# Performance work log

Hardware: AMD Instinct MI355X
Metric: run time of the kernel (lower is better)

## Reference

```python
import jax, jax.numpy as jnp
import numpy as np

B, N, L = 64, 256, 2048
COMP, PROT, GAT, HEADS, LATENT = 128, 128, 64, 4, 128
N_ATOM, N_AMINO = 100, 25
WINDOW, LAYER_CNN, LAYER_OUT = 5, 3, 3
ALPHA = 0.2
BIDAT = 4


def _lrelu(x, s=ALPHA):
    return jax.nn.leaky_relu(x, negative_slope=s)


def _gat(h, adj_pos, W, a, concat):
    # e[b,i,j] = leakyrelu(a1.Wh_i + a2.Wh_j): avoids the O(N^2,2F) concat tensor.
    Wh = h @ W                      # [B,N,F]
    F = W.shape[1]
    f1 = Wh @ a[:F]                 # [B,N]
    f2 = Wh @ a[F:]                 # [B,N]
    e = _lrelu(f1[:, :, None] + f2[:, None, :])          # [B,N,N]
    att = jax.nn.softmax(jnp.where(adj_pos, e, -9e15), axis=2)
    hp = att @ Wh                   # [B,N,F]
    return jax.nn.elu(hp) if concat else hp


def _mask_softmax(a, mask):
    e = jnp.exp(a - jnp.max(a, axis=-1, keepdims=True)) * mask
    return e / (jnp.sum(e, axis=-1, keepdims=True) + 1e-6)


def _forward(atoms, atoms_mask, adjacency, amino, amino_mask, fps, inv_Temp, Temp,
             E_atom, E_amino, gatW, gatA, goW, goA, Wc_w, Wc_b, conv_k, conv_b,
             Wp_w, Wp_b, fp0, fp1, U, t_c2p_w, t_c2p_b, t_p2c_w, t_p2c_b,
             bh_c_w, bh_c_b, bh_p_w, bh_p_b, ba_c_w, ba_c_b, ba_p_w, ba_p_b,
             comb_c_w, comb_c_b, comb_p_w, comb_p_b, Wout_w, Wout_b, out_w, out_b):
    adj_pos = adjacency > 0
    # ---- comp_gat ----
    av = E_atom[atoms]                                   # [B,N,COMP]
    mh = jnp.concatenate([_gat(av, adj_pos, gatW[i], gatA[i], True) for i in range(HEADS)], axis=2)
    av = jax.nn.elu(_gat(mh, adj_pos, goW, goA, False))
    av = _lrelu(av @ Wc_w + Wc_b)                        # [B,N,LATENT]
    # ---- prot_cnn ----
    pv = E_amino[amino][:, None]                         # [B,1,L,PROT]
    for i in range(LAYER_CNN):
        pv = _lrelu(jax.lax.conv_general_dilated(
            pv, conv_k[i][None, None], (1, 1),
            [(WINDOW, WINDOW), (WINDOW, WINDOW)],
            dimension_numbers=("NCHW", "OIHW", "NCHW")) + conv_b[i])
    pv = _lrelu(pv[:, 0] @ Wp_w + Wp_b)                  # [B,L,LATENT]
    # ---- fingerprint superfeature ----
    sf = _lrelu(_lrelu(fps @ fp0, 0.1) @ fp1, 0.1)       # [B,LATENT]
    # ---- bidirectional attention ----
    cfs, pfs = [], []
    for i in range(BIDAT):
        A = jnp.tanh(jnp.einsum("bnd,de,bme->bnm", av, U[i], pv))   # [B,N,L]
        A = A * (atoms_mask[:, :, None] * amino_mask[:, None, :])
        atoms_trans = A @ jnp.tanh(pv @ t_p2c_w[i] + t_p2c_b[i])     # [B,N,LATENT]
        amino_trans = jnp.einsum("bnm,bnd->bmd", A, jnp.tanh(av @ t_c2p_w[i] + t_c2p_b[i]))
        atoms_tmp = jnp.concatenate([jnp.tanh(av @ bh_c_w[i] + bh_c_b[i]), atoms_trans], axis=2)
        amino_tmp = jnp.concatenate([jnp.tanh(pv @ bh_p_w[i] + bh_p_b[i]), amino_trans], axis=2)
        a_att = _mask_softmax((atoms_tmp @ ba_c_w[i] + ba_c_b[i])[..., 0], atoms_mask)
        p_att = _mask_softmax((amino_tmp @ ba_p_w[i] + ba_p_b[i])[..., 0], amino_mask)
        cfs.append(jnp.sum(av * a_att[:, :, None], axis=1))
        pfs.append(jnp.sum(pv * p_att[:, :, None], axis=1))
    cf_final = jnp.concatenate([jnp.concatenate(cfs, axis=1) @ comb_c_w + comb_c_b, sf], axis=1)
    pf_final = jnp.concatenate(pfs, axis=1) @ comb_p_w + comb_p_b
    v = jnp.concatenate([cf_final, pf_final, inv_Temp, Temp], axis=1)   # [B,3*LATENT+2]
    for j in range(LAYER_OUT):
        v = _lrelu(v @ Wout_w[j] + Wout_b[j])
    return v @ out_w + out_b                             # [B,1]


def setup_inputs() -> dict:
    key = jax.random.key(0)
    ks = iter(jax.random.split(key, 48))
    def nrm(shape, scale=0.1):
        return jax.random.normal(next(ks), shape, jnp.float32) * scale
    inp = {}
    inp["atoms"] = jax.random.randint(next(ks), (B, N), 0, N_ATOM)
    inp["atoms_mask"] = jnp.ones((B, N), jnp.float32)
    inp["adjacency"] = jax.random.randint(next(ks), (B, N, N), 0, 2).astype(jnp.int32)
    inp["amino"] = jax.random.randint(next(ks), (B, L), 0, N_AMINO)
    inp["amino_mask"] = jnp.ones((B, L), jnp.float32)
    inp["fps"] = jax.random.uniform(next(ks), (B, 1024), jnp.float32)
    inp["inv_Temp"] = jax.random.uniform(next(ks), (B, 1), jnp.float32)
    inp["Temp"] = jax.random.uniform(next(ks), (B, 1), jnp.float32)
    inp["E_atom"] = nrm((N_ATOM + 1, COMP))
    inp["E_amino"] = nrm((N_AMINO + 1, PROT))
    inp["gatW"] = nrm((HEADS, COMP, GAT))
    inp["gatA"] = nrm((HEADS, 2 * GAT))
    inp["goW"] = nrm((GAT * HEADS, COMP))
    inp["goA"] = nrm((2 * COMP,))
    inp["Wc_w"] = nrm((COMP, LATENT)); inp["Wc_b"] = nrm((LATENT,))
    K = 2 * WINDOW + 1
    inp["conv_k"] = nrm((LAYER_CNN, K, K)); inp["conv_b"] = nrm((LAYER_CNN,))
    inp["Wp_w"] = nrm((PROT, LATENT)); inp["Wp_b"] = nrm((LATENT,))
    inp["fp0"] = nrm((1024, LATENT)); inp["fp1"] = nrm((LATENT, LATENT))
    inp["U"] = nrm((BIDAT, LATENT, LATENT))
    inp["t_c2p_w"] = nrm((BIDAT, LATENT, LATENT)); inp["t_c2p_b"] = nrm((BIDAT, LATENT))
    inp["t_p2c_w"] = nrm((BIDAT, LATENT, LATENT)); inp["t_p2c_b"] = nrm((BIDAT, LATENT))
    inp["bh_c_w"] = nrm((BIDAT, LATENT, LATENT)); inp["bh_c_b"] = nrm((BIDAT, LATENT))
    inp["bh_p_w"] = nrm((BIDAT, LATENT, LATENT)); inp["bh_p_b"] = nrm((BIDAT, LATENT))
    inp["ba_c_w"] = nrm((BIDAT, 2 * LATENT, 1)); inp["ba_c_b"] = nrm((BIDAT, 1))
    inp["ba_p_w"] = nrm((BIDAT, 2 * LATENT, 1)); inp["ba_p_b"] = nrm((BIDAT, 1))
    inp["comb_c_w"] = nrm((BIDAT * LATENT, LATENT)); inp["comb_c_b"] = nrm((LATENT,))
    inp["comb_p_w"] = nrm((BIDAT * LATENT, LATENT)); inp["comb_p_b"] = nrm((LATENT,))
    D = 3 * LATENT + 2
    inp["Wout_w"] = nrm((LAYER_OUT, D, D)); inp["Wout_b"] = nrm((LAYER_OUT, D))
    inp["out_w"] = nrm((D, 1)); inp["out_b"] = nrm((1,))
    return inp


def reference(atoms, atoms_mask, adjacency, amino, amino_mask, fps, inv_Temp, Temp,
              E_atom, E_amino, gatW, gatA, goW, goA, Wc_w, Wc_b, conv_k, conv_b,
              Wp_w, Wp_b, fp0, fp1, U, t_c2p_w, t_c2p_b, t_p2c_w, t_p2c_b,
              bh_c_w, bh_c_b, bh_p_w, bh_p_b, ba_c_w, ba_c_b, ba_p_w, ba_p_b,
              comb_c_w, comb_c_b, comb_p_w, comb_p_b, Wout_w, Wout_b, out_w, out_b):
    return _forward(atoms, atoms_mask, adjacency, amino, amino_mask, fps, inv_Temp, Temp,
                    E_atom, E_amino, gatW, gatA, goW, goA, Wc_w, Wc_b, conv_k, conv_b,
                    Wp_w, Wp_b, fp0, fp1, U, t_c2p_w, t_c2p_b, t_p2c_w, t_p2c_b,
                    bh_c_w, bh_c_b, bh_p_w, bh_p_b, ba_c_w, ba_c_b, ba_p_w, ba_p_b,
                    comb_c_w, comb_c_b, comb_p_w, comb_p_b, Wout_w, Wout_b, out_w, out_b)
```

## Files before the change

### kernel.cpp

```cpp
#include <hip/hip_runtime.h>
#include <math.h>

#define Bn   64
#define Nn   256
#define Ln   2048
#define CMP  128
#define PROT 128
#define GF   64
#define NHEADS 4
#define LT   128
#define DOUT 386
#define CB   32
#define NCH  (Bn / CB)
#define FLSP 4

typedef unsigned short u16;
typedef unsigned long long u64;
typedef __attribute__((ext_vector_type(8))) short short8v;
typedef __attribute__((ext_vector_type(4))) float f32x4;
typedef __attribute__((ext_vector_type(4))) unsigned short u16x4;
typedef __attribute__((ext_vector_type(4))) unsigned int u32x4;

#define MFMA(a, b, c) __builtin_amdgcn_mfma_f32_16x16x32_bf16((a), (b), (c), 0, 0, 0)

__device__ __forceinline__ float apply_act(float v, int act) {
  if (act == 1) return v > 0.f ? v : 0.2f * v;
  if (act == 2) return v > 0.f ? v : 0.1f * v;
  if (act == 3) return tanhf(v);
  return v;
}

__device__ __forceinline__ u16 bfc(float f) {
  union { float f; unsigned u; } x; x.f = f;
  unsigned r = x.u + 0x7fffu + ((x.u >> 16) & 1u);
  return (u16)(r >> 16);
}

__device__ __forceinline__ float bf2f(u16 h) {
  union { unsigned u; float f; } x; x.u = ((unsigned)h) << 16; return x.f;
}

__device__ __forceinline__ float ftanh(float x) {
  float e = __builtin_amdgcn_exp2f(x * 2.885390081777927f);
  return 1.f - 2.f * __builtin_amdgcn_rcpf(e + 1.f);
}

template<int C>
__device__ __forceinline__ int lofs(int r, int c) {
  if (C == 256) return ((r * C + c) * 2) ^ ((r & 15) << 4);
  if (C == 128) return ((r * C + c) * 2) ^ ((r & 15) << 4);
  return ((r * C + c) * 2) ^ ((r & 7) << 4);
}

__device__ __forceinline__ short8v ldsv(const u16* s, int byteofs) {
  return *(const short8v*)((const char*)s + byteofs);
}

__global__ void embed_kernel(const int* __restrict__ idx, const float* __restrict__ E,
                             float* __restrict__ out, long total, int C) {
  long i = (long)blockIdx.x * blockDim.x + threadIdx.x;
  if (i >= total) return;
  long r = i / C;
  int c = (int)(i - r * (long)C);
  out[i] = E[(long)idx[r] * C + c];
}

__global__ void zero_kernel(float* __restrict__ a, long n) {
  long i = (long)blockIdx.x * blockDim.x + threadIdx.x;
  if (i < n) a[i] = 0.f;
}

__global__ void packadj_kernel(const int* __restrict__ adj, u64* __restrict__ adjb) {
  long idx = (long)blockIdx.x * 256 + threadIdx.x;
  int lane = threadIdx.x & 63;
  bool bit = adj[idx] > 0;
  u64 m = __ballot(bit);
  if (lane == 0) adjb[idx >> 6] = m;
}

__global__ void transp_kernel(const float* __restrict__ src, u16* __restrict__ dst,
                              int K, int N) {
  long total = (long)K * N;
  long base = (long)blockIdx.y * total;
  long idx = (long)blockIdx.x * 256 + threadIdx.x;
  if (idx >= total) return;
  int k = (int)(idx % K);
  int n = (int)(idx / K);
  dst[base + idx] = bfc(src[base + (long)k * N + n]);
}

struct Ptr8 { const float* p[8]; };
__global__ void transp8_kernel(Ptr8 srcs, u16* __restrict__ dst) {
  int y = blockIdx.y;
  int idx = blockIdx.x * 256 + threadIdx.x;
  int k = idx & 127, n = idx >> 7;
  dst[(long)y * 16384 + idx] = bfc(srcs.p[y][k * 128 + n]);
}

__global__ void wvec_kernel(const float* __restrict__ gatW, const float* __restrict__ gatA,
                            const float* __restrict__ goW, const float* __restrict__ goA,
                            float* __restrict__ wv) {
  int idx = blockIdx.x * 256 + threadIdx.x;
  if (idx < 1024) {
    int h = idx >> 8, wq = (idx >> 7) & 1, d = idx & 127;
    const float* W = gatW + ((long)h * 128 + d) * 64;
    const float* a = gatA + h * 128 + wq * 64;
    float s = 0.f;
    for (int f = 0; f < 64; ++f) s += W[f] * a[f];
    wv[idx] = s;
  } else if (idx < 1536) {
    int k = idx - 1024; int wq = k >> 8, d = k & 255;
    const float* W = goW + (long)d * 128;
    const float* a = goA + wq * 128;
    float s = 0.f;
    for (int f = 0; f < 128; ++f) s += W[f] * a[f];
    wv[idx] = s;
  }
}

__global__ __launch_bounds__(256) void favv_kernel(
    const float* __restrict__ AVE, const float* __restrict__ wv,
    float* __restrict__ f1, float* __restrict__ f2, long rows)
{
  __shared__ float w[1024];
  int tid = threadIdx.x;
  for (int q = tid; q < 1024; q += 256) w[q] = wv[q];
  __syncthreads();
  long r = (long)blockIdx.x * 4 + (tid >> 6);
  int lane = tid & 63;
  float a0 = AVE[r * 128 + lane], a1 = AVE[r * 128 + 64 + lane];
#pragma unroll
  for (int h = 0; h < 4; ++h) {
    float s1 = a0 * w[h * 256 + lane] + a1 * w[h * 256 + 64 + lane];
    float s2 = a0 * w[h * 256 + 128 + lane] + a1 * w[h * 256 + 192 + lane];
#pragma unroll
    for (int m = 32; m; m >>= 1) { s1 += __shfl_xor(s1, m, 64); s2 += __shfl_xor(s2, m, 64); }
    if (lane == 0) { f1[(long)h * rows + r] = s1; f2[(long)h * rows + r] = s2; }
  }
}

__global__ __launch_bounds__(256) void fmh_kernel(
    const float* __restrict__ MH, const float* __restrict__ gv,
    float* __restrict__ f1, float* __restrict__ f2, long rows)
{
  __shared__ float w[512];
  int tid = threadIdx.x;
  for (int q = tid; q < 512; q += 256) w[q] = gv[q];
  __syncthreads();
  long r = (long)blockIdx.x * 4 + (tid >> 6);
  int lane = tid & 63;
  const float* m = MH + r * 256;
  float s1 = 0.f, s2 = 0.f;
#pragma unroll
  for (int t = 0; t < 4; ++t) {
    float a = m[t * 64 + lane];
    s1 += a * w[t * 64 + lane];
    s2 += a * w[256 + t * 64 + lane];
  }
#pragma unroll
  for (int mm = 32; mm; mm >>= 1) { s1 += __shfl_xor(s1, mm, 64); s2 += __shfl_xor(s2, mm, 64); }
  if (lane == 0) { f1[r] = s1; f2[r] = s2; }
}

__global__ void pack_kernel(
    const float* __restrict__ bh_c_b, const float* __restrict__ t_c2p_b,
    const float* __restrict__ ba_c_w, const float* __restrict__ ba_c_b,
    const float* __restrict__ ba_p_w, const float* __restrict__ bh_p_b,
    const float* __restrict__ t_p2c_b, const float* __restrict__ ba_p_b,
    float* __restrict__ pk_a, float* __restrict__ pk_p)
{
  int idx = blockIdx.x * 256 + threadIdx.x;
  if (idx < 1024) {
    int g = idx >> 7, j = idx & 127;
    pk_a[idx] = g < 4 ? bh_c_b[g * 128 + j] : t_c2p_b[(g - 4) * 128 + j];
    pk_p[idx] = g < 4 ? bh_p_b[g * 128 + j] : t_p2c_b[(g - 4) * 128 + j];
  } else if (idx < 2048) {
    int k = idx - 1024; int g = k >> 7, j = k & 127;
    pk_a[idx] = g < 4 ? ba_c_w[g * 256 + j] : ba_p_w[(g - 4) * 256 + 128 + j];
    pk_p[idx] = g < 4 ? ba_p_w[g * 256 + j] : ba_c_w[(g - 4) * 256 + 128 + j];
  } else if (idx < 2056) {
    int g = idx - 2048;
    pk_a[idx] = g < 4 ? ba_c_b[g] : 0.f;
    pk_p[idx] = g < 4 ? ba_p_b[g] : 0.f;
  }
}

template<int ACT, int OUT>
__global__ __launch_bounds__(256) void mfma_mm_kernel(
    const float* __restrict__ A, const u16* __restrict__ Bt,
    const float* __restrict__ bias, void* __restrict__ Cp,
    int M, int N, int K, int lda, int ldc, int colOff,
    int MBc, long BSt, int ldt)
{
  __shared__ u16 sA[64 * 64];
  __shared__ u16 sB[64 * 64];
  int m0 = blockIdx.y * 64, n0 = blockIdx.x * 64;
  int tid = threadIdx.x, lane = tid & 63, wv = tid >> 6;
  int mh = wv >> 1, nh = wv & 1;
  f32x4 acc00 = {0.f,0.f,0.f,0.f};
  f32x4 acc01 = acc00, acc10 = acc00, acc11 = acc00;
  for (int k0 = 0; k0 < K; k0 += 64) {
#pragma unroll
    for (int q = tid; q < 64 * 16; q += 256) {
      int r = q >> 4, c4 = (q & 15) << 2;
      float4 v = *(const float4*)(A + (long)(m0 + r) * lda + k0 + c4);
      u16x4 h = { bfc(v.x), bfc(v.y), bfc(v.z), bfc(v.w) };
      *(u16x4*)((char*)sA + lofs<64>(r, c4)) = h;
    }
#pragma unroll
    for (int q = tid; q < 64 * 8; q += 256) {
      int r = q >> 3, c8 = (q & 7) << 3;
      *(u32x4*)((char*)sB + lofs<64>(r, c8)) =
          *(const u32x4*)(Bt + (long)(n0 + r) * K + k0 + c8);
    }
    __syncthreads();
#pragma unroll
    for (int kk = 0; kk < 64; kk += 32) {
      int kf = kk + ((lane >> 4) << 3);
      short8v a0 = ldsv(sA, lofs<64>(mh * 32 + (lane & 15), kf));
      short8v a1 = ldsv(sA, lofs<64>(mh * 32 + 16 + (lane & 15), kf));
      short8v b0 = ldsv(sB, lofs<64>(nh * 32 + (lane & 15), kf));
      short8v b1 = ldsv(sB, lofs<64>(nh * 32 + 16 + (lane & 15), kf));
      acc00 = MFMA(a0, b0, acc00);
      acc01 = MFMA(a0, b1, acc01);
      acc10 = MFMA(a1, b0, acc10);
      acc11 = MFMA(a1, b1, acc11);
    }
    __syncthreads();
  }
#pragma unroll
  for (int rt = 0; rt < 2; ++rt) {
#pragma unroll
    for (int ct = 0; ct < 2; ++ct) {
      f32x4 a = rt == 0 ? (ct == 0 ? acc00 : acc01) : (ct == 0 ? acc10 : acc11);
      int col = n0 + nh * 32 + ct * 16 + (lane & 15);
      float bv = bias ? bias[col] : 0.f;
#pragma unroll
      for (int r4 = 0; r4 < 4; ++r4) {
        int row = m0 + mh * 32 + rt * 16 + ((lane >> 4) << 2) + r4;
        float v = apply_act(a[r4] + bv, ACT);
        if (OUT == 0)
          ((float*)Cp)[(long)row * ldc + colOff + col] = v;
        else if (OUT == 1)
          ((u16*)Cp)[(long)row * ldc + col] = bfc(v);
        else
          ((u16*)Cp)[(long)(row / MBc) * BSt + (long)col * ldt + (row % MBc)] = bfc(v);
      }
    }
  }
}

template<int ACT, int OUT>
static void mmx(hipStream_t st, const float* A, const u16* Bt, const float* bias,
                void* C, int M, int N, int K, int lda, int ldc, int colOff = 0,
                int MBc = 1, long BSt = 0, int ldt = 0)
{
  dim3 grid(N / 64, M / 64);
  mfma_mm_kernel<ACT, OUT><<<grid, dim3(256), 0, st>>>(
      A, Bt, bias, C, M, N, K, lda, ldc, colOff, MBc, BSt, ldt);
}

template<int XBF>
__global__ __launch_bounds__(256) void mmdot_kernel(
    const void* __restrict__ Xp, const u16* __restrict__ Wcat,
    const float* __restrict__ pk, float* __restrict__ out, long M)
{
  __shared__ u16 sX[128 * 128];
  __shared__ u16 sW[64 * 128];
  __shared__ float bv_s[64], aw_s[64];
  long m0 = (long)blockIdx.x * 128;
  int g0 = blockIdx.y * 4;
  int tid = threadIdx.x, lane = tid & 63, wv = tid >> 6;
  if (XBF) {
    const u16* X = (const u16*)Xp;
    for (int q = tid; q < 128 * 16; q += 256) {
      int r = q >> 4, c8 = (q & 15) << 3;
      *(u32x4*)((char*)sX + lofs<128>(r, c8)) =
          *(const u32x4*)(X + (m0 + r) * 128 + c8);
    }
  } else {
    const float* X = (const float*)Xp;
    for (int q = tid; q < 128 * 32; q += 256) {
      int r = q >> 5, c4 = (q & 31) << 2;
      float4 v = *(const float4*)(X + (m0 + r) * 128 + c4);
      u16x4 h = { bfc(v.x), bfc(v.y), bfc(v.z), bfc(v.w) };
      *(u16x4*)((char*)sX + lofs<128>(r, c4)) = h;
    }
  }
  for (int gi = 0; gi < 4; ++gi) {
    int g = g0 + gi;
    float p[2][4] = {{0.f,0.f,0.f,0.f},{0.f,0.f,0.f,0.f}};
    for (int hh = 0; hh < 2; ++hh) {
      __syncthreads();
      for (int q = tid; q < 64 * 16; q += 256) {
        int r = q >> 4, c8 = (q & 15) << 3;
        *(u32x4*)((char*)sW + lofs<128>(r, c8)) =
            *(const u32x4*)(Wcat + (long)g * 16384 + (long)(hh * 64 + r) * 128 + c8);
      }
      if (tid < 64) {
        bv_s[tid] = pk[g * 128 + hh * 64 + tid];
        aw_s[tid] = pk[1024 + g * 128 + hh * 64 + tid];
      }
      __syncthreads();
      for (int lt = 0; lt < 4; ++lt) {
        int col = lt * 16 + (lane & 15);
        float bv = bv_s[col], awv = aw_s[col];
#pragma unroll
        for (int rt = 0; rt < 2; ++rt) {
          f32x4 c = {0.f,0.f,0.f,0.f};
#pragma unroll
          for (int kk = 0; kk < 128; kk += 32) {
            int kf = kk + ((lane >> 4) << 3);
            short8v a = ldsv(sX, lofs<128>(wv * 32 + rt * 16 + (lane & 15), kf));
            short8v bb = ldsv(sW, lofs<128>(lt * 16 + (lane & 15), kf));
            c = MFMA(a, bb, c);
          }
#pragma unroll
          for (int r4 = 0; r4 < 4; ++r4)
            p[rt][r4] += ftanh(c[r4] + bv) * awv;
        }
      }
    }
    float ab = pk[2048 + g];
#pragma unroll
    for (int rt = 0; rt < 2; ++rt)
#pragma unroll
      for (int r4 = 0; r4 < 4; ++r4) {
        float s = p[rt][r4];
        s += __shfl_xor(s, 1, 64); s += __shfl_xor(s, 2, 64);
        s += __shfl_xor(s, 4, 64); s += __shfl_xor(s, 8, 64);
        if ((lane & 15) == 0) {
          long row = m0 + wv * 32 + rt * 16 + ((lane >> 4) << 2) + r4;
          out[(long)g * M + row] = s + ab;
        }
      }
  }
}

__global__ __launch_bounds__(256) void bidat_fused(
    const u16* __restrict__ AVU4,
    const u16* __restrict__ PVbf,
    float* __restrict__ OUTP,
    float* __restrict__ OUTA,
    const float* __restrict__ am, const float* __restrict__ pm)
{
  __shared__ u16 sK[128 * 128];
  __shared__ float qm_s[128], pm_s[128], amr_s[128], am_sh[128];
  __shared__ float scp_red[4][128];
  const long NBt = (long)Bn * Nn, LBt = (long)Bn * Ln;
  int b = blockIdx.y;
  int n0 = blockIdx.x * 128;
  int zz = blockIdx.z;
  int it = zz & 3, lz = zz >> 2;
  const float* qv = OUTP + (long)(4 + it) * LBt;
  const float* rv = OUTA + (long)(4 + it) * NBt;
  float* SCA = OUTA + (long)it * NBt;
  float* SCP = OUTP + (long)it * LBt;
  int tid = threadIdx.x, lane = tid & 63, wv = tid >> 6;

  short8v af[2][4];
  {
    long rbase = (long)b * Nn + n0 + wv * 32 + (lane & 15);
    int cbase = it * 128 + ((lane >> 4) << 3);
#pragma unroll
    for (int rt = 0; rt < 2; ++rt)
#pragma unroll
      for (int k4 = 0; k4 < 4; ++k4)
        af[rt][k4] = *(const short8v*)(AVU4 + (rbase + rt * 16) * 512 + cbase + k4 * 32);
  }
  if (tid < 128) {
    float amv = am[(long)b * Nn + n0 + tid];
    am_sh[tid] = amv;
    amr_s[tid] = amv * rv[(long)b * Nn + n0 + tid];
  }
  float sca_r[2][4] = {{0.f,0.f,0.f,0.f},{0.f,0.f,0.f,0.f}};
  const u16* pvb = PVbf + (long)b * Ln * 128;
  int lbeg = lz * (Ln / FLSP);

  for (int l0 = lbeg; l0 < lbeg + Ln / FLSP; l0 += 128) {
    __syncthreads();
    for (int q = tid; q < 128 * 16; q += 256) {
      int r = q >> 4, c8 = (q & 15) << 3;
      *(u32x4*)((char*)sK + lofs<128>(r, c8)) =
          *(const u32x4*)(pvb + (long)(l0 + r) * 128 + c8);
    }
    if (tid < 128) {
      float pmv = pm[(long)b * Ln + l0 + tid];
      pm_s[tid] = pmv;
      qm_s[tid] = pmv * qv[(long)b * Ln + l0 + tid];
    }
    __syncthreads();
    for (int lt = 0; lt < 8; ++lt) {
      float sp = 0.f;
      float qmv = qm_s[lt * 16 + (lane & 15)];
#pragma unroll
      for (int rt = 0; rt < 2; ++rt) {
        f32x4 c = {0.f,0.f,0.f,0.f};
#pragma unroll
        for (int k4 = 0; k4 < 4; ++k4) {
          short8v bb = ldsv(sK, lofs<128>(lt * 16 + (lane & 15),
                                          k4 * 32 + ((lane >> 4) << 3)));
          c = MFMA(af[rt][k4], bb, c);
        }
#pragma unroll
        for (int r4 = 0; r4 < 4; ++r4) {
          int nr = wv * 32 + rt * 16 + ((lane >> 4) << 2) + r4;
          float t = ftanh(c[r4]);
          sca_r[rt][r4] += t * qmv;
          sp += t * amr_s[nr];
        }
      }
      sp += __shfl_xor(sp, 16, 64);
      sp += __shfl_xor(sp, 32, 64);
      if (lane < 16) scp_red[wv][lt * 16 + lane] = sp;
    }
    __syncthreads();
    if (tid < 128) {
      float v = scp_red[0][tid] + scp_red[1][tid] + scp_red[2][tid] + scp_red[3][tid];
      atomicAdd(&SCP[(long)b * Ln + l0 + tid], v * pm_s[tid]);
    }
  }
#pragma unroll
  for (int rt = 0; rt < 2; ++rt)
#pragma unroll
    for (int r4 = 0; r4 < 4; ++r4) {
      float s = sca_r[rt][r4];
      s += __shfl_xor(s, 1, 64); s += __shfl_xor(s, 2, 64);
      s += __shfl_xor(s, 4, 64); s += __shfl_xor(s, 8, 64);
      if ((lane & 15) == 0) {
        int nr = wv * 32 + rt * 16 + ((lane >> 4) << 2) + r4;
        atomicAdd(&SCA[(long)b * Nn + n0 + nr], s * am_sh[nr]);
      }
    }
}

__global__ __launch_bounds__(256) void mm_kernel(
    const float* __restrict__ A, const float* __restrict__ Bm,
    const float* __restrict__ bias, float* __restrict__ C,
    int M, int N, int K, int lda, int ldb, int ldc, int colOff, int act)
{
  __shared__ float As[32][33];
  __shared__ float Bs[32][33];
  int tx = threadIdx.x, ty = threadIdx.y;
  int tid = ty * 16 + tx;
  int m0 = blockIdx.y * 32;
  int n0 = blockIdx.x * 32;
  float acc00 = 0.f, acc01 = 0.f, acc10 = 0.f, acc11 = 0.f;
  for (int k0 = 0; k0 < K; k0 += 32) {
#pragma unroll
    for (int t = 0; t < 4; ++t) {
      int li = tid + t * 256;
      int r = li >> 5, c = li & 31;
      int mm = m0 + r, kk = k0 + c;
      As[r][c] = (mm < M && kk < K) ? A[(long)mm * lda + kk] : 0.f;
      int kk2 = k0 + r, nn = n0 + c;
      Bs[r][c] = (kk2 < K && nn < N) ? Bm[(long)kk2 * ldb + nn] : 0.f;
    }
    __syncthreads();
#pragma unroll
    for (int kk = 0; kk < 32; ++kk) {
      float a0 = As[ty][kk], a1 = As[ty + 16][kk];
      float b0 = Bs[kk][tx], b1 = Bs[kk][tx + 16];
      acc00 += a0 * b0; acc01 += a0 * b1;
      acc10 += a1 * b0; acc11 += a1 * b1;
    }
    __syncthreads();
  }
  float accs[2][2] = {{acc00, acc01}, {acc10, acc11}};
#pragma unroll
  for (int i = 0; i < 2; ++i) {
    int m = m0 + ty + i * 16;
    if (m >= M) continue;
#pragma unroll
    for (int j = 0; j < 2; ++j) {
      int n = n0 + tx + j * 16;
      if (n >= N) continue;
      float v = accs[i][j];
      if (bias) v += bias[n];
      C[(long)m * ldc + colOff + n] = apply_act(v, act);
    }
  }
}

static void mm(hipStream_t st, const float* A, const float* Bm, const float* bias,
               float* C, int M, int N, int K, int lda, int ldb, int ldc,
               int colOff, int act)
{
  dim3 grid((N + 31) / 32, (M + 31) / 32), block(16, 16);
  mm_kernel<<<grid, block, 0, st>>>(A, Bm, bias, C, M, N, K, lda, ldb, ldc, colOff, act);
}

template<int F>
__global__ __launch_bounds__(256) void gat3_kernel(
    const u16* __restrict__ WhT, long bStride,
    const float* __restrict__ f1, const float* __restrict__ f2,
    const u64* __restrict__ adjb,
    float* __restrict__ out, int ldo)
{
  __shared__ u16 sP[32 * 256];
  __shared__ u16 sW[F * 32];
  __shared__ float f2s[256];
  __shared__ float f1s[32], mrow[32], srow[32];
  __shared__ u64 adjm[32][4];
  int b = blockIdx.y, i0 = blockIdx.x * 32, h = blockIdx.z;
  int tid = threadIdx.x, lane = tid & 63, wv = tid >> 6;
  const long rowb = (long)b * Nn;
  const float* f1h = f1 + (long)h * Bn * Nn;
  const float* f2h = f2 + (long)h * Bn * Nn;

  if (tid < 32) f1s[tid] = f1h[rowb + i0 + tid];
  f2s[tid] = f2h[rowb + tid];
  if (tid < 128) adjm[tid >> 2][tid & 3] = adjb[(rowb + i0 + (tid >> 2)) * 4 + (tid & 3)];
  __syncthreads();

  {
    int r = tid >> 3, s = tid & 7;
    float f1v = f1s[r];
    float mx = -3.4e38f;
    for (int j = s; j < 256; j += 8) {
      bool bit = (adjm[r][j >> 6] >> (j & 63)) & 1;
      float e = f1v + f2s[j]; e = e > 0.f ? e : 0.2f * e;
      mx = fmaxf(mx, bit ? e : -9e15f);
    }
    mx = fmaxf(mx, __shfl_xor(mx, 1, 64));
    mx = fmaxf(mx, __shfl_xor(mx, 2, 64));
    mx = fmaxf(mx, __shfl_xor(mx, 4, 64));
    float sum = 0.f;
    for (int j = s; j < 256; j += 8) {
      bool bit = (adjm[r][j >> 6] >> (j & 63)) & 1;
      float e = f1v + f2s[j]; e = e > 0.f ? e : 0.2f * e;
      sum += __expf((bit ? e : -9e15f) - mx);
    }
    sum += __shfl_xor(sum, 1, 64);
    sum += __shfl_xor(sum, 2, 64);
    sum += __shfl_xor(sum, 4, 64);
    if (s == 0) { mrow[r] = mx; srow[r] = 1.f / sum; }
  }
  __syncthreads();
  {
    int j = tid;
    float f2v = f2s[j];
    int w64 = j >> 6, sh = j & 63;
    for (int r = 0; r < 32; ++r) {
      bool bit = (adjm[r][w64] >> sh) & 1;
      float e = f1s[r] + f2v; e = e > 0.f ? e : 0.2f * e;
      float p = __expf((bit ? e : -9e15f) - mrow[r]);
      *(u16*)((char*)sP + lofs<256>(r, j)) = bfc(p);
    }
  }
  constexpr int NT = F / 32;
  f32x4 acc[NT];
#pragma unroll
  for (int t = 0; t < NT; ++t) acc[t] = f32x4{0.f,0.f,0.f,0.f};
  const u16* Wb = WhT + (long)b * bStride + (long)h * F * 256;
  int mh = wv & 1;
  for (int k0 = 0; k0 < 256; k0 += 32) {
    __syncthreads();
    for (int q = tid; q < F * 4; q += 256) {
      int n = q >> 2, c8 = (q & 3) << 3;
      *(u32x4*)((char*)sW + ((n * 64 + c8 * 2) ^ ((n & 7) << 4))) =
          *(const u32x4*)(Wb + (long)n * 256 + k0 + c8);
    }
    __syncthreads();
    int kf = (lane >> 4) << 3;
    short8v a = ldsv(sP, lofs<256>(mh * 16 + (lane & 15), k0 + kf));
#pragma unroll
    for (int t = 0; t < NT; ++t) {
      int n = ((wv >> 1) * NT + t) * 16 + (lane & 15);
      short8v bb = *(const short8v*)((char*)sW + ((n * 64 + kf * 2) ^ ((n & 7) << 4)));
      acc[t] = MFMA(a, bb, acc[t]);
    }
  }
#pragma unroll
  for (int t = 0; t < NT; ++t) {
    int col = ((wv >> 1) * NT + t) * 16 + (lane & 15);
#pragma unroll
    for (int r4 = 0; r4 < 4; ++r4) {
      int rl = mh * 16 + ((lane >> 4) << 2) + r4;
      float v = acc[t][r4] * srow[rl];
      v = v > 0.f ? v : expm1f(v);
      out[(rowb + i0 + rl) * (long)ldo + h * F + col] = v;
    }
  }
}

__global__ __launch_bounds__(128) void conv11_kernel(
    const float* __restrict__ in, const float* __restrict__ kw,
    const float* __restrict__ bias_p, float* __restrict__ out)
{
  __shared__ float s[26][140];
  __shared__ float kk[121];
  int b = blockIdx.y;
  int l0 = blockIdx.x * 16;
  int tid = threadIdx.x;
  if (tid < 121) kk[tid] = kw[tid];
  const float* inb = in + (long)b * Ln * PROT;
  for (int r = 0; r < 26; ++r) {
    int l = l0 - 5 + r;
    for (int c = tid; c < 138; c += 128) {
      int p = c - 5;
      float v = 0.f;
      if (l >= 0 && l < Ln && p >= 0 && p < PROT) v = inb[(long)l * PROT + p];
      s[r][c] = v;
    }
  }
  __syncthreads();
  float bias = bias_p[0];
  float acc[16];
#pragma unroll
  for (int i = 0; i < 16; ++i) acc[i] = bias;
  int p = tid;
#pragma unroll
  for (int v = 0; v < 11; ++v) {
    float c[26];
#pragma unroll
    for (int u = 0; u < 26; ++u) c[u] = s[u][p + v];
#pragma unroll
    for (int u = 0; u < 11; ++u) {
      float w = kk[u * 11 + v];
#pragma unroll
      for (int i = 0; i < 16; ++i) acc[i] += c[i + u] * w;
    }
  }
  float* outb = out + (long)b * Ln * PROT;
#pragma unroll
  for (int i = 0; i < 16; ++i) {
    float vv = acc[i];
    outb[(long)(l0 + i) * PROT + p] = vv > 0.f ? vv : 0.2f * vv;
  }
}

__global__ __launch_bounds__(128) void conv11e_kernel(
    const int* __restrict__ amino, const float* __restrict__ E,
    const float* __restrict__ kw, const float* __restrict__ bias_p,
    float* __restrict__ out)
{
  __shared__ float s[26][140];
  __shared__ float kk[121];
  int b = blockIdx.y;
  int l0 = blockIdx.x * 16;
  int tid = threadIdx.x;
  if (tid < 121) kk[tid] = kw[tid];
  const int* amb = amino + (long)b * Ln;
  for (int r = 0; r < 26; ++r) {
    int l = l0 - 5 + r;
    int idx = (l >= 0 && l < Ln) ? amb[l] : -1;
    const float* Er = E + (long)(idx < 0 ? 0 : idx) * PROT;
    for (int c = tid; c < 138; c += 128) {
      int p = c - 5;
      float v = 0.f;
      if (idx >= 0 && p >= 0 && p < PROT) v = Er[p];
      s[r][c] = v;
    }
  }
  __syncthreads();
  float bias = bias_p[0];
  float acc[16];
#pragma unroll
  for (int i = 0; i < 16; ++i) acc[i] = bias;
  int p = tid;
#pragma unroll
  for (int v = 0; v < 11; ++v) {
    float c[26];
#pragma unroll
    for (int u = 0; u < 26; ++u) c[u] = s[u][p + v];
#pragma unroll
    for (int u = 0; u < 11; ++u) {
      float w = kk[u * 11 + v];
#pragma unroll
      for (int i = 0; i < 16; ++i) acc[i] += c[i + u] * w;
    }
  }
  float* outb = out + (long)b * Ln * PROT;
#pragma unroll
  for (int i = 0; i < 16; ++i) {
    float vv = acc[i];
    outb[(long)(l0 + i) * PROT + p] = vv > 0.f ? vv : 0.2f * vv;
  }
}

__global__ __launch_bounds__(256) void mask_softmax_kernel(
    const float* __restrict__ score, const float* __restrict__ mask,
    float* __restrict__ att, int n)
{
  int b = blockIdx.x;
  long st = (long)blockIdx.y * gridDim.x * n;
  int tid = threadIdx.x;
  __shared__ float red[256];
  const float* s = score + st + (long)b * n;
  const float* mk = mask + (long)b * n;
  float mx = -3.4e38f;
  for (int i = tid; i < n; i += 256) mx = fmaxf(mx, s[i]);
  red[tid] = mx; __syncthreads();
  for (int stp = 128; stp > 0; stp >>= 1) { if (tid < stp) red[tid] = fmaxf(red[tid], red[tid + stp]); __syncthreads(); }
  mx = red[0]; __syncthreads();
  float sum = 0.f;
  for (int i = tid; i < n; i += 256) sum += __expf(s[i] - mx) * mk[i];
  red[tid] = sum; __syncthreads();
  for (int stp = 128; stp > 0; stp >>= 1) { if (tid < stp) red[tid] += red[tid + stp]; __syncthreads(); }
  float denom = red[0] + 1e-6f;
  for (int i = tid; i < n; i += 256)
    att[st + (long)b * n + i] = __expf(s[i] - mx) * mk[i] / denom;
}

template<int XBF>
__global__ __launch_bounds__(128) void wsum_kernel(
    const void* __restrict__ xp, const float* __restrict__ att,
    float* __restrict__ out, int n, int nsplit)
{
  int b = blockIdx.x;
  int sp = blockIdx.y;
  int it = blockIdx.z;
  int d = threadIdx.x;
  int chunk = n / nsplit;
  int t0 = sp * chunk, t1 = t0 + chunk;
  const float* ab = att + (long)it * gridDim.x * n + (long)b * n;
  float acc = 0.f;
  if (XBF) {
    const u16* xb = (const u16*)xp + (long)b * n * LT + d;
#pragma unroll 8
    for (int t = t0; t < t1; ++t) acc += bf2f(xb[(long)t * LT]) * ab[t];
  } else {
    const float* xb = (const float*)xp + (long)b * n * LT + d;
#pragma unroll 8
    for (int t = t0; t < t1; ++t) acc += xb[(long)t * LT] * ab[t];
  }
  atomicAdd(&out[(long)b * 512 + it * LT + d], acc);
}

__global__ __launch_bounds__(128) void assemble_v_kernel(
    const float* __restrict__ sf, const float* __restrict__ invT,
    const float* __restrict__ T, float* __restrict__ v)
{
  int b = blockIdx.x;
  int t = threadIdx.x;
  v[(long)b * DOUT + 128 + t] = sf[(long)b * LT + t];
  if (t == 0) { v[(long)b * DOUT + 384] = invT[b]; v[(long)b * DOUT + 385] = T[b]; }
}

extern "C" void kernel_launch(void* const* d_in, const int* in_sizes, int n_in,
                              void* d_out, int out_size, void* d_ws, size_t ws_size,
                              hipStream_t stream) {
  const long NB = (long)Bn * Nn;
  const long LB = (long)Bn * Ln;
  const long M1 = 1024 * 1024;

  const int*   atoms      = (const int*)d_in[0];
  const float* atoms_mask = (const float*)d_in[1];
  const int*   adj        = (const int*)d_in[2];
  const int*   amino      = (const int*)d_in[3];
  const float* amino_mask = (const float*)d_in[4];
  const float* fps        = (const float*)d_in[5];
  const float* invT       = (const float*)d_in[6];
  const float* Temp       = (const float*)d_in[7];
  const float* E_atom     = (const float*)d_in[8];
  const float* E_amino    = (const float*)d_in[9];
  const float* gatW       = (const float*)d_in[10];
  const float* gatA       = (const float*)d_in[11];
  const float* goW        = (const float*)d_in[12];
  const float* goA        = (const float*)d_in[13];
  const float* Wc_w       = (const float*)d_in[14];
  const float* Wc_b       = (const float*)d_in[15];
  const float* conv_k     = (const float*)d_in[16];
  const float* conv_b     = (const float*)d_in[17];
  const float* Wp_w       = (const float*)d_in[18];
  const float* Wp_b       = (const float*)d_in[19];
  const float* fp0        = (const float*)d_in[20];
  const float* fp1        = (const float*)d_in[21];
  const float* U          = (const float*)d_in[22];
  const float* t_c2p_w    = (const float*)d_in[23];
  const float* t_c2p_b    = (const float*)d_in[24];
  const float* t_p2c_w    = (const float*)d_in[25];
  const float* t_p2c_b    = (const float*)d_in[26];
  const float* bh_c_w     = (const float*)d_in[27];
  const float* bh_c_b     = (const float*)d_in[28];
  const float* bh_p_w     = (const float*)d_in[29];
  const float* bh_p_b     = (const float*)d_in[30];
  const float* ba_c_w     = (const float*)d_in[31];
  const float* ba_c_b     = (const float*)d_in[32];
  const float* ba_p_w     = (const float*)d_in[33];
  const float* ba_p_b     = (const float*)d_in[34];
  const float* comb_c_w   = (const float*)d_in[35];
  const float* comb_c_b   = (const float*)d_in[36];
  const float* comb_p_w   = (const float*)d_in[37];
  const float* comb_p_b   = (const float*)d_in[38];
  const float* Wout_w     = (const float*)d_in[39];
  const float* Wout_b     = (const float*)d_in[40];
  const float* out_w      = (const float*)d_in[41];
  const float* out_b      = (const float*)d_in[42];
  float* out = (float*)d_out;

  float* ws = (float*)d_ws;
  long off = 0;
  float* AV    = ws + off; off += NB * LT;
  u16*   PVbf  = (u16*)(ws + off); off += LB * LT / 2;
  float* SF    = ws + off; off += (long)Bn * LT;
  float* SFT   = ws + off; off += (long)Bn * LT;
  float* CF    = ws + off; off += (long)Bn * 512;
  float* PF    = ws + off; off += (long)Bn * 512;
  float* F1    = ws + off; off += 4 * NB;
  float* F2    = ws + off; off += 4 * NB;
  float* ATTA4 = ws + off; off += 4 * NB;
  float* ATTP4 = ws + off; off += 4 * LB;
  float* V0    = ws + off; off += (long)Bn * DOUT;
  float* V1    = ws + off; off += (long)Bn * DOUT;
  u64*   ADJB  = (u64*)(ws + off); off += NB * 4 * 2;
  float* WVEC  = ws + off; off += 2048;
  u16* WT = (u16*)(ws + off);
  long wo = 0;
  u16* gatW_t  = WT + wo; wo += 4L * 64 * 128;
  u16* goW_t   = WT + wo; wo += 128L * 256;
  u16* T23     = WT + wo; wo += 23L * 16384;
  u16* fp0_t   = WT + wo; wo += 128L * 1024;
  u16* combc_t = WT + wo; wo += 128L * 512;
  u16* combp_t = WT + wo; wo += 128L * 512;
  off += (wo + 1) / 2;
  float* pk_a = ws + off; off += 2056;
  float* pk_p = ws + off; off += 2056;
  float* POOL = ws + off;
  u16* Wc_t   = T23;
  u16* Wp_t   = T23 + 16384;
  u16* fp1_t  = T23 + 2L * 16384;
  u16* U_t    = T23 + 3L * 16384;
  u16* wcat_a = T23 + 7L * 16384;
  u16* wcat_p = T23 + 15L * 16384;
  float* AVE   = POOL;
  u16*   WhT4  = (u16*)(POOL + 2 * M1);
  float* MH    = POOL + 4 * M1;
  u16*   WhT2  = (u16*)POOL;
  float* G2    = POOL + 2 * M1;
  float* PVA   = POOL;
  float* PVB   = POOL + 8 * M1;
  u16*   AVU4  = (u16*)POOL;
  float* OUTP  = POOL + 4 * M1;
  float* OUTA  = POOL + 5 * M1;

  transp_kernel<<<dim3(32, 4), 256, 0, stream>>>(gatW, gatW_t, 128, 64);
  transp_kernel<<<dim3(128), 256, 0, stream>>>(goW, goW_t, 256, 128);
  transp_kernel<<<dim3(512), 256, 0, stream>>>(fp0, fp0_t, 1024, 128);
  transp_kernel<<<dim3(256), 256, 0, stream>>>(comb_c_w, combc_t, 512, 128);
  transp_kernel<<<dim3(256), 256, 0, stream>>>(comb_p_w, combp_t, 512, 128);
  {
    Ptr8 a1 = {{Wc_w, Wp_w, fp1, U, U + 16384, U + 32768, U + 49152, bh_c_w}};
    Ptr8 a2 = {{bh_c_w + 16384, bh_c_w + 32768, bh_c_w + 49152,
                t_c2p_w, t_c2p_w + 16384, t_c2p_w + 32768, t_c2p_w + 49152,
                bh_p_w}};
    Ptr8 a3 = {{bh_p_w + 16384, bh_p_w + 32768, bh_p_w + 49152,
                t_p2c_w, t_p2c_w + 16384, t_p2c_w + 32768, t_p2c_w + 49152,
                bh_p_w}};
    transp8_kernel<<<dim3(64, 8), 256, 0, stream>>>(a1, T23);
    transp8_kernel<<<dim3(64, 8), 256, 0, stream>>>(a2, T23 + 8L * 16384);
    transp8_kernel<<<dim3(64, 7), 256, 0, stream>>>(a3, T23 + 16L * 16384);
  }
  pack_kernel<<<dim3(9), 256, 0, stream>>>(bh_c_b, t_c2p_b, ba_c_w, ba_c_b,
                                           ba_p_w, bh_p_b, t_p2c_b, ba_p_b,
                                           pk_a, pk_p);
  packadj_kernel<<<dim3((unsigned)(NB * Nn / 256)), 256, 0, stream>>>(adj, ADJB);
  wvec_kernel<<<dim3(6), 256, 0, stream>>>(gatW, gatA, goW, goA, WVEC);

  embed_kernel<<<dim3((unsigned)((NB * CMP + 255) / 256)), 256, 0, stream>>>(
      atoms, E_atom, AVE, NB * CMP, CMP);
  mmx<0, 2>(stream, AVE, gatW_t, nullptr, WhT4, (int)NB, 256, 128, 128, 0, 0,
            256, 256L * 256, 256);
  favv_kernel<<<dim3((unsigned)(NB / 4)), 256, 0, stream>>>(AVE, WVEC, F1, F2, NB);
  gat3_kernel<GF><<<dim3(Nn / 32, Bn, 4), 256, 0, stream>>>(
      WhT4, 256L * 256, F1, F2, ADJB, MH, 256);
  mmx<0, 2>(stream, MH, goW_t, nullptr, WhT2, (int)NB, 128, 256, 256, 0, 0,
            256, 128L * 256, 256);
  fmh_kernel<<<dim3((unsigned)(NB / 4)), 256, 0, stream>>>(MH, WVEC + 1024, F1, F2, NB);
  gat3_kernel<CMP><<<dim3(Nn / 32, Bn, 1), 256, 0, stream>>>(
      WhT2, 128L * 256, F1, F2, ADJB, G2, 128);
  mmx<1, 0>(stream, G2, Wc_t, Wc_b, AV, (int)NB, 128, 128, 128, 128);

  for (int c = 0; c < NCH; ++c) {
    long b0 = (long)c * CB;
    conv11e_kernel<<<dim3(Ln / 16, CB), 128, 0, stream>>>(
        amino + b0 * Ln, E_amino, conv_k + 0 * 121, conv_b + 0, PVA);
    conv11_kernel<<<dim3(Ln / 16, CB), 128, 0, stream>>>(PVA, conv_k + 1 * 121, conv_b + 1, PVB);
    conv11_kernel<<<dim3(Ln / 16, CB), 128, 0, stream>>>(PVB, conv_k + 2 * 121, conv_b + 2, PVA);
    mmx<1, 1>(stream, PVA, Wp_t, Wp_b, PVbf + b0 * Ln * 128,
              (int)((long)CB * Ln), 128, 128, 128, 128);
  }

  mmx<2, 0>(stream, fps, fp0_t, nullptr, SFT, Bn, 128, 1024, 1024, 128);
  mmx<2, 0>(stream, SFT, fp1_t, nullptr, SF, Bn, 128, 128, 128, 128);

  mmdot_kernel<1><<<dim3((unsigned)(LB / 128), 2), 256, 0, stream>>>(
      PVbf, wcat_p, pk_p, OUTP, LB);
  mmdot_kernel<0><<<dim3((unsigned)(NB / 128), 2), 256, 0, stream>>>(
      AV, wcat_a, pk_a, OUTA, NB);
  mmx<0, 1>(stream, AV, U_t, nullptr, AVU4, (int)NB, 512, 128, 128, 512);
  zero_kernel<<<dim3((unsigned)((2L * Bn * 512 + 255) / 256)), 256, 0, stream>>>(
      CF, 2L * Bn * 512);
  bidat_fused<<<dim3(Nn / 128, Bn, FLSP * 4), 256, 0, stream>>>(
      AVU4, PVbf, OUTP, OUTA, atoms_mask, amino_mask);
  mask_softmax_kernel<<<dim3(Bn, 4), 256, 0, stream>>>(OUTA, atoms_mask, ATTA4, Nn);
  mask_softmax_kernel<<<dim3(Bn, 4), 256, 0, stream>>>(OUTP, amino_mask, ATTP4, Ln);
  wsum_kernel<0><<<dim3(Bn, 8, 4), 128, 0, stream>>>(AV, ATTA4, CF, Nn, 8);
  wsum_kernel<1><<<dim3(Bn, 8, 4), 128, 0, stream>>>(PVbf, ATTP4, PF, Ln, 8);

  mmx<0, 0>(stream, CF, combc_t, comb_c_b, V0, Bn, 128, 512, 512, DOUT, 0);
  mmx<0, 0>(stream, PF, combp_t, comb_p_b, V0, Bn, 128, 512, 512, DOUT, 256);
  assemble_v_kernel<<<Bn, 128, 0, stream>>>(SF, invT, Temp, V0);
  mm(stream, V0, Wout_w,                     Wout_b,            V1, Bn, DOUT, DOUT, DOUT, DOUT, DOUT, 0, 1);
  mm(stream, V1, Wout_w + (long)DOUT * DOUT, Wout_b + DOUT,     V0, Bn, DOUT, DOUT, DOUT, DOUT, DOUT, 0, 1);
  mm(stream, V0, Wout_w + 2L * DOUT * DOUT,  Wout_b + 2 * DOUT, V1, Bn, DOUT, DOUT, DOUT, DOUT, DOUT, 0, 1);
  mm(stream, V1, out_w, out_b, out, Bn, 1, DOUT, DOUT, 1, 1, 0, 0);
}
```

Baseline: 1.194 ms.

## Prefetch weights/K tiles in registers, split GAT transpose store, fuse wsum heads

```diff
diff --git a/kernel.cpp b/kernel.cpp
--- a/kernel.cpp
+++ b/kernel.cpp
@@ -95,6 +95,28 @@
   int idx = blockIdx.x * 256 + threadIdx.x;
   int k = idx & 127, n = idx >> 7;
   dst[(long)y * 16384 + idx] = bfc(srcs.p[y][k * 128 + n]);
+}
+
+__global__ __launch_bounds__(256) void transpT_kernel(
+    const u16* __restrict__ in, u16* __restrict__ out, int C)
+{
+  __shared__ u16 sT[64 * 64];
+  int c0 = blockIdx.x * 64, r0 = blockIdx.y * 64, b = blockIdx.z;
+  int tid = threadIdx.x;
+  for (int q = tid; q < 512; q += 256) {
+    int r = q >> 3, c8 = (q & 7) << 3;
+    *(u32x4*)((char*)sT + lofs<64>(r, c8)) =
+        *(const u32x4*)(in + ((long)b * Nn + r0 + r) * C + c0 + c8);
+  }
+  __syncthreads();
+  int c = tid >> 2, r8 = (tid & 3) << 4;
+  u16 tmp[16];
+#pragma unroll
+  for (int j = 0; j < 16; ++j)
+    tmp[j] = *(const u16*)((char*)sT + lofs<64>(r8 + j, c));
+  long ob = ((long)b * C + c0 + c) * 256 + r0 + r8;
+  *(u32x4*)(out + ob) = *(u32x4*)tmp;
+  *(u32x4*)(out + ob + 8) = *(u32x4*)(tmp + 8);
 }
 
 __global__ void wvec_kernel(const float* __restrict__ gatW, const float* __restrict__ gatA,
@@ -189,8 +211,7 @@
 __global__ __launch_bounds__(256) void mfma_mm_kernel(
     const float* __restrict__ A, const u16* __restrict__ Bt,
     const float* __restrict__ bias, void* __restrict__ Cp,
-    int M, int N, int K, int lda, int ldc, int colOff,
-    int MBc, long BSt, int ldt)
+    int M, int N, int K, int lda, int ldc, int colOff)
 {
   __shared__ u16 sA[64 * 64];
   __shared__ u16 sB[64 * 64];
@@ -241,10 +262,8 @@
         float v = apply_act(a[r4] + bv, ACT);
         if (OUT == 0)
           ((float*)Cp)[(long)row * ldc + colOff + col] = v;
-        else if (OUT == 1)
+        else
           ((u16*)Cp)[(long)row * ldc + col] = bfc(v);
-        else
-          ((u16*)Cp)[(long)(row / MBc) * BSt + (long)col * ldt + (row % MBc)] = bfc(v);
       }
     }
   }
@@ -252,12 +271,11 @@
 
 template<int ACT, int OUT>
 static void mmx(hipStream_t st, const float* A, const u16* Bt, const float* bias,
-                void* C, int M, int N, int K, int lda, int ldc, int colOff = 0,
-                int MBc = 1, long BSt = 0, int ldt = 0)
+                void* C, int M, int N, int K, int lda, int ldc, int colOff = 0)
 {
   dim3 grid(N / 64, M / 64);
   mfma_mm_kernel<ACT, OUT><<<grid, dim3(256), 0, st>>>(
-      A, Bt, bias, C, M, N, K, lda, ldc, colOff, MBc, BSt, ldt);
+      A, Bt, bias, C, M, N, K, lda, ldc, colOff);
 }
 
 template<int XBF>
@@ -287,53 +305,72 @@
       *(u16x4*)((char*)sX + lofs<128>(r, c4)) = h;
     }
   }
-  for (int gi = 0; gi < 4; ++gi) {
-    int g = g0 + gi;
-    float p[2][4] = {{0.f,0.f,0.f,0.f},{0.f,0.f,0.f,0.f}};
-    for (int hh = 0; hh < 2; ++hh) {
-      __syncthreads();
-      for (int q = tid; q < 64 * 16; q += 256) {
-        int r = q >> 4, c8 = (q & 15) << 3;
-        *(u32x4*)((char*)sW + lofs<128>(r, c8)) =
-            *(const u32x4*)(Wcat + (long)g * 16384 + (long)(hh * 64 + r) * 128 + c8);
+  int rj[4], cj[4];
+#pragma unroll
+  for (int j = 0; j < 4; ++j) { int q = tid + j * 256; rj[j] = q >> 4; cj[j] = (q & 15) << 3; }
+  u32x4 wpf[4];
+  float bvp = 0.f, awp = 0.f;
+  {
+#pragma unroll
+    for (int j = 0; j < 4; ++j)
+      wpf[j] = *(const u32x4*)(Wcat + (long)g0 * 16384 + (long)rj[j] * 128 + cj[j]);
+    if (tid < 64) { bvp = pk[g0 * 128 + tid]; awp = pk[1024 + g0 * 128 + tid]; }
+  }
+  float p[2][4];
+  for (int s = 0; s < 8; ++s) {
+    int gi = s >> 1, hh = s & 1, g = g0 + gi;
+    if (hh == 0) {
+#pragma unroll
+      for (int rt = 0; rt < 2; ++rt)
+#pragma unroll
+        for (int r4 = 0; r4 < 4; ++r4) p[rt][r4] = 0.f;
+    }
+    __syncthreads();
+#pragma unroll
+    for (int j = 0; j < 4; ++j)
+      *(u32x4*)((char*)sW + lofs<128>(rj[j], cj[j])) = wpf[j];
+    if (tid < 64) { bv_s[tid] = bvp; aw_s[tid] = awp; }
+    if (s < 7) {
+      int s2 = s + 1, g2 = g0 + (s2 >> 1), h2 = s2 & 1;
+#pragma unroll
+      for (int j = 0; j < 4; ++j)
+        wpf[j] = *(const u32x4*)(Wcat + (long)g2 * 16384 + (long)(h2 * 64 + rj[j]) * 128 + cj[j]);
+      if (tid < 64) { bvp = pk[g2 * 128 + h2 * 64 + tid]; awp = pk[1024 + g2 * 128 + h2 * 64 + tid]; }
+    }
+    __syncthreads();
+    for (int lt = 0; lt < 4; ++lt) {
+      int col = lt * 16 + (lane & 15);
+      float bv = bv_s[col], awv = aw_s[col];
+#pragma unroll
+      for (int rt = 0; rt < 2; ++rt) {
+        f32x4 c = {0.f,0.f,0.f,0.f};
+#pragma unroll
+        for (int kk = 0; kk < 128; kk += 32) {
+          int kf = kk + ((lane >> 4) << 3);
+          short8v a = ldsv(sX, lofs<128>(wv * 32 + rt * 16 + (lane & 15), kf));
+          short8v bb = ldsv(sW, lofs<128>(lt * 16 + (lane & 15), kf));
+          c = MFMA(a, bb, c);
+        }
+#pragma unroll
+        for (int r4 = 0; r4 < 4; ++r4)
+          p[rt][r4] += ftanh(c[r4] + bv) * awv;
       }
-      if (tid < 64) {
-        bv_s[tid] = pk[g * 128 + hh * 64 + tid];
-        aw_s[tid] = pk[1024 + g * 128 + hh * 64 + tid];
-      }
-      __syncthreads();
-      for (int lt = 0; lt < 4; ++lt) {
-        int col = lt * 16 + (lane & 15);
-        float bv = bv_s[col], awv = aw_s[col];
-#pragma unroll
-        for (int rt = 0; rt < 2; ++rt) {
-          f32x4 c = {0.f,0.f,0.f,0.f};
-#pragma unroll
-          for (int kk = 0; kk < 128; kk += 32) {
-            int kf = kk + ((lane >> 4) << 3);
-            short8v a = ldsv(sX, lofs<128>(wv * 32 + rt * 16 + (lane & 15), kf));
-            short8v bb = ldsv(sW, lofs<128>(lt * 16 + (lane & 15), kf));
-            c = MFMA(a, bb, c);
+    }
+    if (hh == 1) {
+      float ab = pk[2048 + g];
+#pragma unroll
+      for (int rt = 0; rt < 2; ++rt)
+#pragma unroll
+        for (int r4 = 0; r4 < 4; ++r4) {
+          float sv = p[rt][r4];
+          sv += __shfl_xor(sv, 1, 64); sv += __shfl_xor(sv, 2, 64);
+          sv += __shfl_xor(sv, 4, 64); sv += __shfl_xor(sv, 8, 64);
+          if ((lane & 15) == 0) {
+            long row = m0 + wv * 32 + rt * 16 + ((lane >> 4) << 2) + r4;
+            out[(long)g * M + row] = sv + ab;
           }
-#pragma unroll
-          for (int r4 = 0; r4 < 4; ++r4)
-            p[rt][r4] += ftanh(c[r4] + bv) * awv;
         }
-      }
-    }
-    float ab = pk[2048 + g];
-#pragma unroll
-    for (int rt = 0; rt < 2; ++rt)
-#pragma unroll
-      for (int r4 = 0; r4 < 4; ++r4) {
-        float s = p[rt][r4];
-        s += __shfl_xor(s, 1, 64); s += __shfl_xor(s, 2, 64);
-        s += __shfl_xor(s, 4, 64); s += __shfl_xor(s, 8, 64);
-        if ((lane & 15) == 0) {
-          long row = m0 + wv * 32 + rt * 16 + ((lane >> 4) << 2) + r4;
-          out[(long)g * M + row] = s + ab;
-        }
-      }
+    }
   }
 }
 
@@ -344,9 +381,9 @@
     float* __restrict__ OUTA,
     const float* __restrict__ am, const float* __restrict__ pm)
 {
-  __shared__ u16 sK[128 * 128];
-  __shared__ float qm_s[128], pm_s[128], amr_s[128], am_sh[128];
-  __shared__ float scp_red[4][128];
+  __shared__ u16 sK[64 * 128];
+  __shared__ float qm_s[64], pm_s[64], amr_s[128], am_sh[128];
+  __shared__ float scp_red[4][64];
   const long NBt = (long)Bn * Nn, LBt = (long)Bn * Ln;
   int b = blockIdx.y;
   int n0 = blockIdx.x * 128;
@@ -357,6 +394,7 @@
   float* SCA = OUTA + (long)it * NBt;
   float* SCP = OUTP + (long)it * LBt;
   int tid = threadIdx.x, lane = tid & 63, wv = tid >> 6;
+  const long bLn = (long)b * Ln;
 
   short8v af[2][4];
   {
@@ -374,23 +412,37 @@
     amr_s[tid] = amv * rv[(long)b * Nn + n0 + tid];
   }
   float sca_r[2][4] = {{0.f,0.f,0.f,0.f},{0.f,0.f,0.f,0.f}};
-  const u16* pvb = PVbf + (long)b * Ln * 128;
+  const u16* pvb = PVbf + bLn * 128;
   int lbeg = lz * (Ln / FLSP);
 
-  for (int l0 = lbeg; l0 < lbeg + Ln / FLSP; l0 += 128) {
-    __syncthreads();
-    for (int q = tid; q < 128 * 16; q += 256) {
-      int r = q >> 4, c8 = (q & 15) << 3;
-      *(u32x4*)((char*)sK + lofs<128>(r, c8)) =
-          *(const u32x4*)(pvb + (long)(l0 + r) * 128 + c8);
-    }
-    if (tid < 128) {
-      float pmv = pm[(long)b * Ln + l0 + tid];
-      pm_s[tid] = pmv;
-      qm_s[tid] = pmv * qv[(long)b * Ln + l0 + tid];
-    }
-    __syncthreads();
-    for (int lt = 0; lt < 8; ++lt) {
+  int rj[4], cj[4];
+#pragma unroll
+  for (int j = 0; j < 4; ++j) { int q = tid + j * 256; rj[j] = q >> 4; cj[j] = (q & 15) << 3; }
+  u32x4 kpf[4];
+  float ppm = 0.f, pqv = 0.f;
+  {
+#pragma unroll
+    for (int j = 0; j < 4; ++j)
+      kpf[j] = *(const u32x4*)(pvb + (long)(lbeg + rj[j]) * 128 + cj[j]);
+    if (tid < 64) { ppm = pm[bLn + lbeg + tid]; pqv = qv[bLn + lbeg + tid]; }
+  }
+
+  for (int ci = 0; ci < (Ln / FLSP) / 64; ++ci) {
+    int l0 = lbeg + ci * 64;
+    __syncthreads();
+#pragma unroll
+    for (int j = 0; j < 4; ++j)
+      *(u32x4*)((char*)sK + lofs<128>(rj[j], cj[j])) = kpf[j];
+    if (tid < 64) { pm_s[tid] = ppm; qm_s[tid] = ppm * pqv; }
+    if (ci + 1 < (Ln / FLSP) / 64) {
+      int ln = l0 + 64;
+#pragma unroll
+      for (int j = 0; j < 4; ++j)
+        kpf[j] = *(const u32x4*)(pvb + (long)(ln + rj[j]) * 128 + cj[j]);
+      if (tid < 64) { ppm = pm[bLn + ln + tid]; pqv = qv[bLn + ln + tid]; }
+    }
+    __syncthreads();
+    for (int lt = 0; lt < 4; ++lt) {
       float sp = 0.f;
       float qmv = qm_s[lt * 16 + (lane & 15)];
 #pragma unroll
@@ -415,9 +467,9 @@
       if (lane < 16) scp_red[wv][lt * 16 + lane] = sp;
     }
     __syncthreads();
-    if (tid < 128) {
+    if (tid < 64) {
       float v = scp_red[0][tid] + scp_red[1][tid] + scp_red[2][tid] + scp_red[3][tid];
-      atomicAdd(&SCP[(long)b * Ln + l0 + tid], v * pm_s[tid]);
+      atomicAdd(&SCP[bLn + l0 + tid], v * pm_s[tid]);
     }
   }
 #pragma unroll
@@ -710,22 +762,30 @@
 {
   int b = blockIdx.x;
   int sp = blockIdx.y;
-  int it = blockIdx.z;
   int d = threadIdx.x;
   int chunk = n / nsplit;
   int t0 = sp * chunk, t1 = t0 + chunk;
-  const float* ab = att + (long)it * gridDim.x * n + (long)b * n;
-  float acc = 0.f;
+  long bn = (long)b * n;
+  long itS = (long)Bn * n;
+  float acc[4] = {0.f, 0.f, 0.f, 0.f};
   if (XBF) {
-    const u16* xb = (const u16*)xp + (long)b * n * LT + d;
-#pragma unroll 8
-    for (int t = t0; t < t1; ++t) acc += bf2f(xb[(long)t * LT]) * ab[t];
+    const u16* xb = (const u16*)xp + bn * LT + d;
+    for (int t = t0; t < t1; ++t) {
+      float xv = bf2f(xb[(long)t * LT]);
+#pragma unroll
+      for (int it = 0; it < 4; ++it) acc[it] += xv * att[it * itS + bn + t];
+    }
   } else {
-    const float* xb = (const float*)xp + (long)b * n * LT + d;
-#pragma unroll 8
-    for (int t = t0; t < t1; ++t) acc += xb[(long)t * LT] * ab[t];
-  }
-  atomicAdd(&out[(long)b * 512 + it * LT + d], acc);
+    const float* xb = (const float*)xp + bn * LT + d;
+    for (int t = t0; t < t1; ++t) {
+      float xv = xb[(long)t * LT];
+#pragma unroll
+      for (int it = 0; it < 4; ++it) acc[it] += xv * att[it * itS + bn + t];
+    }
+  }
+#pragma unroll
+  for (int it = 0; it < 4; ++it)
+    atomicAdd(&out[(long)b * 512 + it * LT + d], acc[it]);
 }
 
 __global__ __launch_bounds__(128) void assemble_v_kernel(
@@ -825,9 +885,11 @@
   u16* wcat_a = T23 + 7L * 16384;
   u16* wcat_p = T23 + 15L * 16384;
   float* AVE   = POOL;
-  u16*   WhT4  = (u16*)(POOL + 2 * M1);
-  float* MH    = POOL + 4 * M1;
-  u16*   WhT2  = (u16*)POOL;
+  u16*   WhRM4 = (u16*)(POOL + 2 * M1);
+  u16*   WhT4  = (u16*)(POOL + 4 * M1);
+  float* MH    = POOL + 6 * M1;
+  u16*   WhRM2 = (u16*)POOL;
+  u16*   WhT2  = (u16*)(POOL + 1 * M1);
   float* G2    = POOL + 2 * M1;
   float* PVA   = POOL;
   float* PVB   = POOL + 8 * M1;
@@ -860,13 +922,13 @@
 
   embed_kernel<<<dim3((unsigned)((NB * CMP + 255) / 256)), 256, 0, stream>>>(
       atoms, E_atom, AVE, NB * CMP, CMP);
-  mmx<0, 2>(stream, AVE, gatW_t, nullptr, WhT4, (int)NB, 256, 128, 128, 0, 0,
-            256, 256L * 256, 256);
+  mmx<0, 1>(stream, AVE, gatW_t, nullptr, WhRM4, (int)NB, 256, 128, 128, 256);
+  transpT_kernel<<<dim3(4, 4, Bn), 256, 0, stream>>>(WhRM4, WhT4, 256);
   favv_kernel<<<dim3((unsigned)(NB / 4)), 256, 0, stream>>>(AVE, WVEC, F1, F2, NB);
   gat3_kernel<GF><<<dim3(Nn / 32, Bn, 4), 256, 0, stream>>>(
       WhT4, 256L * 256, F1, F2, ADJB, MH, 256);
-  mmx<0, 2>(stream, MH, goW_t, nullptr, WhT2, (int)NB, 128, 256, 256, 0, 0,
-            256, 128L * 256, 256);
+  mmx<0, 1>(stream, MH, goW_t, nullptr, WhRM2, (int)NB, 128, 256, 256, 128);
+  transpT_kernel<<<dim3(2, 4, Bn), 256, 0, stream>>>(WhRM2, WhT2, 128);
   fmh_kernel<<<dim3((unsigned)(NB / 4)), 256, 0, stream>>>(MH, WVEC + 1024, F1, F2, NB);
   gat3_kernel<CMP><<<dim3(Nn / 32, Bn, 1), 256, 0, stream>>>(
       WhT2, 128L * 256, F1, F2, ADJB, G2, 128);
@@ -896,8 +958,8 @@
       AVU4, PVbf, OUTP, OUTA, atoms_mask, amino_mask);
   mask_softmax_kernel<<<dim3(Bn, 4), 256, 0, stream>>>(OUTA, atoms_mask, ATTA4, Nn);
   mask_softmax_kernel<<<dim3(Bn, 4), 256, 0, stream>>>(OUTP, amino_mask, ATTP4, Ln);
-  wsum_kernel<0><<<dim3(Bn, 8, 4), 128, 0, stream>>>(AV, ATTA4, CF, Nn, 8);
-  wsum_kernel<1><<<dim3(Bn, 8, 4), 128, 0, stream>>>(PVbf, ATTP4, PF, Ln, 8);
+  wsum_kernel<0><<<dim3(Bn, 4), 128, 0, stream>>>(AV, ATTA4, CF, Nn, 4);
+  wsum_kernel<1><<<dim3(Bn, 16), 128, 0, stream>>>(PVbf, ATTP4, PF, Ln, 16);
 
   mmx<0, 0>(stream, CF, combc_t, comb_c_b, V0, Bn, 128, 512, 512, DOUT, 0);
   mmx<0, 0>(stream, PF, combp_t, comb_p_b, V0, Bn, 128, 512, 512, DOUT, 256);
```

Result: slower. 1.285 ms (+7.6%).
